# Optimization experiments

Measured on AMD Instinct MI355X. Metric: run time of the kernel, lower is better.

Reference implementation:

```python
import jax, jax.numpy as jnp
import numpy as np

B, L, H, O, NL = 1024, 100, 256, 256, 2


def setup_inputs() -> dict:
    key = jax.random.key(0)
    ks = jax.random.split(key, 20)
    s = 0.05  # weight scale to keep gates/softmax well-conditioned
    d = {
        "encoder_outputs": jax.random.normal(ks[0], (B, L, H), jnp.float32),
        "enc_h": jax.random.normal(ks[1], (NL, B, H), jnp.float32),
        "enc_c": jax.random.normal(ks[2], (NL, B, H), jnp.float32),
        "embedding": jax.random.uniform(ks[3], (O, H), jnp.float32, -1.0, 1.0),
        # torch nn.LSTM params, gate order (i, f, g, o)
        "Wih0": jax.random.normal(ks[4], (4 * H, 2 * H), jnp.float32) * s,
        "Whh0": jax.random.normal(ks[5], (4 * H, H), jnp.float32) * s,
        "bih0": jax.random.normal(ks[6], (4 * H,), jnp.float32) * s,
        "bhh0": jax.random.normal(ks[7], (4 * H,), jnp.float32) * s,
        "Wih1": jax.random.normal(ks[8], (4 * H, H), jnp.float32) * s,
        "Whh1": jax.random.normal(ks[9], (4 * H, H), jnp.float32) * s,
        "bih1": jax.random.normal(ks[10], (4 * H,), jnp.float32) * s,
        "bhh1": jax.random.normal(ks[11], (4 * H,), jnp.float32) * s,
        "Wa": jax.random.normal(ks[12], (H, H), jnp.float32) * s,        # Luong general score
        "Wconcat": jax.random.normal(ks[13], (H, 2 * H), jnp.float32) * s,
        "Wout": jax.random.normal(ks[14], (O, H), jnp.float32) * s,
        "Wcrit": jax.random.normal(ks[15], (O, O), jnp.float32) * s,
        "bcrit": jax.random.normal(ks[16], (O,), jnp.float32) * s,
        "actions": jax.random.randint(ks[17], (B, L), 0, O, jnp.int32),
    }
    return d


def _lstm_cell(x, h, c, Wih, Whh, bih, bhh):
    gates = x @ Wih.T + h @ Whh.T + bih + bhh  # [B, 4H]
    i, f, g, o = jnp.split(gates, 4, axis=-1)
    i = jax.nn.sigmoid(i)
    f = jax.nn.sigmoid(f)
    g = jnp.tanh(g)
    o = jax.nn.sigmoid(o)
    c_new = f * c + i * g
    h_new = o * jnp.tanh(c_new)
    return h_new, c_new


def reference(encoder_outputs, enc_h, enc_c, embedding,
              Wih0, Whh0, bih0, bhh0, Wih1, Whh1, bih1, bhh1,
              Wa, Wconcat, Wout, Wcrit, bcrit, actions):
    # Precompute Luong 'general' projection of encoder states (same math each step)
    enc_proj = encoder_outputs @ Wa.T  # [B, L, H]

    def step(carry, act_t):
        x, h, c, ctx = carry  # x:[B] int, h/c:[NL,B,H], ctx:[B,H]
        emb = embedding[x]                               # [B, H]
        inp = jnp.concatenate([emb, ctx], axis=-1)       # [B, 2H]
        h0, c0 = _lstm_cell(inp, h[0], c[0], Wih0, Whh0, bih0, bhh0)
        h1, c1 = _lstm_cell(h0, h[1], c[1], Wih1, Whh1, bih1, bhh1)
        out = h1                                         # [B, H]
        scores = jnp.einsum('bh,blh->bl', out, enc_proj)  # Luong general score
        attn = jax.nn.softmax(scores, axis=-1)
        ctx_att = jnp.einsum('bl,blh->bh', attn, encoder_outputs)
        new_ctx = jnp.tanh(jnp.concatenate([out, ctx_att], axis=-1) @ Wconcat.T)  # [B, H]
        logit_raw = new_ctx @ Wout.T                     # [B, O]
        pi = jax.nn.softmax(logit_raw, axis=-1)
        Q = logit_raw @ Wcrit.T + bcrit
        new_carry = (act_t, jnp.stack([h0, h1]), jnp.stack([c0, c1]), new_ctx)
        return new_carry, (pi, Q)

    x0 = jnp.zeros((B,), jnp.int32)
    ctx0 = encoder_outputs.mean(axis=1)                  # [B, H]
    _, (pis, Qs) = jax.lax.scan(step, (x0, enc_h, enc_c, ctx0), actions.T)
    logits = jnp.transpose(pis, (1, 0, 2))               # [B, L, O] (softmax probs, as in torch code)
    qvalues = jnp.transpose(Qs, (1, 0, 2))               # [B, L, O]
    values = (qvalues * logits).sum(-1)                  # [B, L]
    decoder_action = actions.astype(jnp.float32)         # teacher-forced actions recorded per step
    return decoder_action, logits, values
```

## Files before the change

### kernel.cpp

```cpp
#include <hip/hip_runtime.h>


#define Bx 1024
#define Lq 100
#define Hd 256
#define Od 256
#define H4 1024

typedef _Float16 f16;
typedef _Float16 half2_t __attribute__((ext_vector_type(2)));
typedef _Float16 f16x4 __attribute__((ext_vector_type(4)));
typedef unsigned int uint;
typedef uint uint4v __attribute__((ext_vector_type(4)));

__device__ __forceinline__ float fdot2(half2_t a, half2_t b, float c) {
#if __has_builtin(__builtin_amdgcn_fdot2)
  return __builtin_amdgcn_fdot2(a, b, c, false);
#else
  return c + (float)a.x * (float)b.x + (float)a.y * (float)b.y;
#endif
}
__device__ __forceinline__ float dot8(float acc, float4 w, float4 a) {
  acc = fdot2(__builtin_bit_cast(half2_t, w.x), __builtin_bit_cast(half2_t, a.x), acc);
  acc = fdot2(__builtin_bit_cast(half2_t, w.y), __builtin_bit_cast(half2_t, a.y), acc);
  acc = fdot2(__builtin_bit_cast(half2_t, w.z), __builtin_bit_cast(half2_t, a.z), acc);
  acc = fdot2(__builtin_bit_cast(half2_t, w.w), __builtin_bit_cast(half2_t, a.w), acc);
  return acc;
}
__device__ __forceinline__ float sigmf(float x) { return 1.0f / (1.0f + __expf(-x)); }



__global__ void k_cvt_lstm(const float* Wih0, const float* Whh0,
                           const float* Wih1, const float* Whh1, f16* dst) {
  int row = blockIdx.x, seg = row >> 10, r = row & 1023, c = threadIdx.x;
  const float* src; int stride, off;
  if (seg == 0)      { src = Wih0; stride = 512; off = 256; }
  else if (seg == 1) { src = Whh0; stride = 256; off = 0; }
  else if (seg == 2) { src = Wih1; stride = 256; off = 0; }
  else               { src = Whh1; stride = 256; off = 0; }
  size_t didx = (size_t)seg * 262144 + (size_t)(r >> 6) * 16384 +
                (size_t)(c >> 3) * 512 + (size_t)(r & 63) * 8 + (c & 7);
  dst[didx] = (f16)src[(size_t)r * stride + off + c];
}

__global__ void k_cvt_small(const float* Wconcat, const float* Wout,
                            const float* Wcrit, const float* Wa, f16* dst) {
  int blk = blockIdx.x, seg = blk >> 8, r = blk & 255, c = threadIdx.x;
  if (seg == 0) {
    dst[(size_t)(r >> 6) * 32768 + (size_t)(c >> 3) * 512 + (r & 63) * 8 + (c & 7)] =
        (f16)Wconcat[(size_t)r * 512 + c];
    int c2 = c + 256;
    dst[(size_t)(r >> 6) * 32768 + (size_t)(c2 >> 3) * 512 + (r & 63) * 8 + (c2 & 7)] =
        (f16)Wconcat[(size_t)r * 512 + c2];
  } else if (seg == 1) {
    dst[131072 + (size_t)(r >> 6) * 16384 + (size_t)(c >> 3) * 512 + (r & 63) * 8 + (c & 7)] =
        (f16)Wout[(size_t)r * 256 + c];
  } else if (seg == 2) {
    dst[196608 + (size_t)(r >> 6) * 16384 + (size_t)(c >> 3) * 512 + (r & 63) * 8 + (c & 7)] =
        (f16)Wcrit[(size_t)r * 256 + c];
  } else {
    dst[262144 + (size_t)(c >> 6) * 16384 + (size_t)(r >> 3) * 512 + (c & 63) * 8 + (r & 7)] =
        (f16)Wa[(size_t)r * 256 + c];
  }
}

__global__ void k_bias1(const float* bih1, const float* bhh1, float* b1) {
  int i = blockIdx.x * 256 + threadIdx.x;
  b1[i] = bih1[i] + bhh1[i];
}

__global__ void k_actions(const int* actions, float* out) {
  int i = blockIdx.x * 256 + threadIdx.x;
  out[i] = (float)actions[i];
}

__global__ void k_cvt_enc(const float* enc, f16* dst) {
  size_t i = (size_t)blockIdx.x * 256 + threadIdx.x;
  const float4* s = (const float4*)enc;
  float4 v = s[i];
  f16x4 o = {(f16)v.x, (f16)v.y, (f16)v.z, (f16)v.w};
  *(f16x4*)(dst + 4 * i) = o;
}

__global__ void k_table0(const float* emb, const float* Wih0,
                         const float* bih0, const float* bhh0, float* t0) {
  __shared__ float shw[16][256];
  int j0 = blockIdx.x * 16, tid = threadIdx.x;
  for (int i = tid; i < 16 * 256; i += 256) {
    int r = i >> 8, c = i & 255;
    shw[r][c] = Wih0[(size_t)(j0 + r) * 512 + c];
  }
  __syncthreads();
  int a = tid;
  float acc[16];
#pragma unroll
  for (int r = 0; r < 16; r++) acc[r] = 0.f;
  for (int k = 0; k < 256; k++) {
    float e = emb[(size_t)a * 256 + k];
#pragma unroll
    for (int r = 0; r < 16; r++) acc[r] = fmaf(e, shw[r][k], acc[r]);
  }
#pragma unroll
  for (int r = 0; r < 16; r++)
    t0[(size_t)a * H4 + j0 + r] = acc[r] + bih0[j0 + r] + bhh0[j0 + r];
}

template <bool E16>
__launch_bounds__(1024)
__global__ void k_seq(const float* enc, const f16* enc16,
                      const float* enc_h, const float* enc_c,
                      const int* actions, const float* bcrit,
                      const f16* wWih0c, const f16* wWhh0,
                      const f16* wWih1, const f16* wWhh1,
                      const f16* wWconcat, const f16* wWout, const f16* wWcrit,
                      const f16* wWaT,
                      const float* table0, const float* bias1, float* out) {
  const int tid = threadIdx.x;
  const int b0 = blockIdx.x * 4;

  __shared__ _Float16 sh_h0[4][264];
  __shared__ _Float16 sh_h1[4][264];
  __shared__ _Float16 sh_ctx[4][264];
  __shared__ _Float16 sh_ca[4][264];
  __shared__ _Float16 sh_logit[4][264];
  __shared__ _Float16 sh_v[4][264];
  __shared__ float sh_c0[4][256];
  __shared__ float sh_c1[4][256];
  __shared__ float sh_gates[4][H4];
  __shared__ float sh_sc[4][128];
  __shared__ float sh_pi[4][256];
  __shared__ float sh_red[4][20];
  __shared__ int sh_a[4];

  {
    int bb = tid >> 8, h = tid & 255, gb = b0 + bb;
    sh_h0[bb][h] = (f16)enc_h[(size_t)(0 * Bx + gb) * Hd + h];
    sh_h1[bb][h] = (f16)enc_h[(size_t)(1 * Bx + gb) * Hd + h];
    sh_c0[bb][h] = enc_c[(size_t)(0 * Bx + gb) * Hd + h];
    sh_c1[bb][h] = enc_c[(size_t)(1 * Bx + gb) * Hd + h];
    const float* ep = enc + (size_t)gb * Lq * Hd + h;
    float s = 0.f;
#pragma unroll 4
    for (int l = 0; l < Lq; l++) s += __builtin_nontemporal_load(ep + (size_t)l * Hd);
    sh_ctx[bb][h] = (f16)(s * (1.0f / Lq));
  }
  __syncthreads();

  for (int t = 0; t < Lq; t++) {
    if (tid < 4) sh_a[tid] = (t == 0) ? 0 : actions[(size_t)(b0 + tid) * Lq + (t - 1)];
    __syncthreads();

    {
      const int j = tid;
      const f16* w1 = wWih0c + (size_t)(j >> 6) * 16384 + (j & 63) * 8;
      const f16* w2 = wWhh0 + (size_t)(j >> 6) * 16384 + (j & 63) * 8;
      float a0 = table0[(size_t)sh_a[0] * H4 + j];
      float a1 = table0[(size_t)sh_a[1] * H4 + j];
      float a2 = table0[(size_t)sh_a[2] * H4 + j];
      float a3 = table0[(size_t)sh_a[3] * H4 + j];
#pragma unroll 4
      for (int c = 0; c < 32; c++) {
        float4 wa = *(const float4*)(w1 + (size_t)c * 512);
        float4 wb = *(const float4*)(w2 + (size_t)c * 512);
        float4 x0 = *(const float4*)&sh_ctx[0][8 * c];
        float4 x1 = *(const float4*)&sh_ctx[1][8 * c];
        float4 x2 = *(const float4*)&sh_ctx[2][8 * c];
        float4 x3 = *(const float4*)&sh_ctx[3][8 * c];
        a0 = dot8(a0, wa, x0); a1 = dot8(a1, wa, x1);
        a2 = dot8(a2, wa, x2); a3 = dot8(a3, wa, x3);
        float4 y0 = *(const float4*)&sh_h0[0][8 * c];
        float4 y1 = *(const float4*)&sh_h0[1][8 * c];
        float4 y2 = *(const float4*)&sh_h0[2][8 * c];
        float4 y3 = *(const float4*)&sh_h0[3][8 * c];
        a0 = dot8(a0, wb, y0); a1 = dot8(a1, wb, y1);
        a2 = dot8(a2, wb, y2); a3 = dot8(a3, wb, y3);
      }
      sh_gates[0][j] = a0; sh_gates[1][j] = a1;
      sh_gates[2][j] = a2; sh_gates[3][j] = a3;
    }
    __syncthreads();

    {
      int bb = tid >> 8, h = tid & 255;
      float gi = sh_gates[bb][h], gf = sh_gates[bb][h + 256];
      float gg = sh_gates[bb][h + 512], go = sh_gates[bb][h + 768];
      float c = sigmf(gf) * sh_c0[bb][h] + sigmf(gi) * tanhf(gg);
      sh_c0[bb][h] = c;
      sh_h0[bb][h] = (f16)(sigmf(go) * tanhf(c));
    }
    __syncthreads();

    {
      const int j = tid;
      const f16* w1 = wWih1 + (size_t)(j >> 6) * 16384 + (j & 63) * 8;
      const f16* w2 = wWhh1 + (size_t)(j >> 6) * 16384 + (j & 63) * 8;
      float bv = bias1[j];
      float a0 = bv, a1 = bv, a2 = bv, a3 = bv;
#pragma unroll 4
      for (int c = 0; c < 32; c++) {
        float4 wa = *(const float4*)(w1 + (size_t)c * 512);
        float4 wb = *(const float4*)(w2 + (size_t)c * 512);
        float4 x0 = *(const float4*)&sh_h0[0][8 * c];
        float4 x1 = *(const float4*)&sh_h0[1][8 * c];
        float4 x2 = *(const float4*)&sh_h0[2][8 * c];
        float4 x3 = *(const float4*)&sh_h0[3][8 * c];
        a0 = dot8(a0, wa, x0); a1 = dot8(a1, wa, x1);
        a2 = dot8(a2, wa, x2); a3 = dot8(a3, wa, x3);
        float4 y0 = *(const float4*)&sh_h1[0][8 * c];
        float4 y1 = *(const float4*)&sh_h1[1][8 * c];
        float4 y2 = *(const float4*)&sh_h1[2][8 * c];
        float4 y3 = *(const float4*)&sh_h1[3][8 * c];
        a0 = dot8(a0, wb, y0); a1 = dot8(a1, wb, y1);
        a2 = dot8(a2, wb, y2); a3 = dot8(a3, wb, y3);
      }
      sh_gates[0][j] = a0; sh_gates[1][j] = a1;
      sh_gates[2][j] = a2; sh_gates[3][j] = a3;
    }
    __syncthreads();

    {
      int bb = tid >> 8, h = tid & 255;
      float gi = sh_gates[bb][h], gf = sh_gates[bb][h + 256];
      float gg = sh_gates[bb][h + 512], go = sh_gates[bb][h + 768];
      float c = sigmf(gf) * sh_c1[bb][h] + sigmf(gi) * tanhf(gg);
      sh_c1[bb][h] = c;
      sh_h1[bb][h] = (f16)(sigmf(go) * tanhf(c));
    }
    __syncthreads();

    {
      int bb = tid >> 8, h = tid & 255;
      const f16* w = wWaT + (size_t)(h >> 6) * 16384 + (h & 63) * 8;
      float s = 0.f;
#pragma unroll 4
      for (int c = 0; c < 32; c++) {
        float4 wv = *(const float4*)(w + (size_t)c * 512);
        float4 av = *(const float4*)&sh_h1[bb][8 * c];
        s = dot8(s, wv, av);
      }
      sh_v[bb][h] = (f16)s;
    }
    __syncthreads();

    {
      int bb = tid >> 8, l = tid & 255;
      if (l < Lq) {
        float s = 0.f;
        if constexpr (E16) {
          const uint4v* ep = (const uint4v*)(enc16 + ((size_t)(b0 + bb) * Lq + l) * Hd);
#pragma unroll 4
          for (int c = 0; c < 32; c++) {
            uint4v u = ep[c];
            float4 ev = __builtin_bit_cast(float4, u);
            float4 vv = *(const float4*)&sh_v[bb][8 * c];
            s = dot8(s, ev, vv);
          }
        } else {
          const float4* ep = (const float4*)(enc + ((size_t)(b0 + bb) * Lq + l) * Hd);
#pragma unroll 4
          for (int c = 0; c < 64; c++) {
            float4 u = ep[c];
            const f16* vv = &sh_v[bb][4 * c];
            s = fmaf(u.x, (float)vv[0], s);
            s = fmaf(u.y, (float)vv[1], s);
            s = fmaf(u.z, (float)vv[2], s);
            s = fmaf(u.w, (float)vv[3], s);
          }
        }
        sh_sc[bb][l] = s;
      }
    }
    __syncthreads();

    if (tid < 256) {
      int bb = tid >> 6, lane = tid & 63;
      float v0 = (lane < Lq) ? sh_sc[bb][lane] : -1e30f;
      float v1 = (lane + 64 < Lq) ? sh_sc[bb][lane + 64] : -1e30f;
      float m = fmaxf(v0, v1);
      for (int off = 32; off; off >>= 1) m = fmaxf(m, __shfl_xor(m, off));
      float e0 = (lane < Lq) ? __expf(v0 - m) : 0.f;
      float e1 = (lane + 64 < Lq) ? __expf(v1 - m) : 0.f;
      float s = e0 + e1;
      for (int off = 32; off; off >>= 1) s += __shfl_xor(s, off);
      float inv = 1.0f / s;
      if (lane < Lq) sh_sc[bb][lane] = e0 * inv;
      if (lane + 64 < Lq) sh_sc[bb][lane + 64] = e1 * inv;
    }
    __syncthreads();

    if constexpr (E16) {
      int bb = tid >> 8, r = tid & 255;
      int hh = r & 127, half = r >> 7;
      const uint* ep = (const uint*)(enc16 + (size_t)(b0 + bb) * Lq * Hd) + hh;
      float s0 = 0.f, s1 = 0.f;
      int l0 = half * 50;
#pragma unroll 5
      for (int l = l0; l < l0 + 50; l++) {
        uint u = ep[(size_t)l * 128];
        half2_t hv = __builtin_bit_cast(half2_t, u);
        float a = sh_sc[bb][l];
        s0 = fmaf(a, (float)hv.x, s0);
        s1 = fmaf(a, (float)hv.y, s1);
      }
      sh_gates[bb][half * 512 + hh] = s0;
      sh_gates[bb][half * 512 + 128 + hh] = s1;
      __syncthreads();
      if (half == 0) {
        float r0 = sh_gates[bb][hh] + sh_gates[bb][512 + hh];
        float r1 = sh_gates[bb][128 + hh] + sh_gates[bb][512 + 128 + hh];
        half2_t rr = {(f16)r0, (f16)r1};
        *(half2_t*)&sh_ca[bb][2 * hh] = rr;
      }
    } else {
      int bb = tid >> 8, h = tid & 255;
      const float* ep = enc + (size_t)(b0 + bb) * Lq * Hd + h;
      float s = 0.f;
#pragma unroll 4
      for (int l = 0; l < Lq; l++)
        s = fmaf(sh_sc[bb][l], ep[(size_t)l * Hd], s);
      sh_ca[bb][h] = (f16)s;
    }
    __syncthreads();

    {
      int bb = tid >> 8, j = tid & 255;
      const f16* w = wWconcat + (size_t)(j >> 6) * 32768 + (j & 63) * 8;
      float s = 0.f;
#pragma unroll 4
      for (int c = 0; c < 32; c++) {
        float4 wv = *(const float4*)(w + (size_t)c * 512);
        float4 av = *(const float4*)&sh_h1[bb][8 * c];
        s = dot8(s, wv, av);
      }
#pragma unroll 4
      for (int c = 0; c < 32; c++) {
        float4 wv = *(const float4*)(w + (size_t)(32 + c) * 512);
        float4 av = *(const float4*)&sh_ca[bb][8 * c];
        s = dot8(s, wv, av);
      }
      sh_ctx[bb][j] = (f16)tanhf(s);
    }
    __syncthreads();

    {
      int bb = tid >> 8, o = tid & 255;
      const f16* w = wWout + (size_t)(o >> 6) * 16384 + (o & 63) * 8;
      float s = 0.f;
#pragma unroll 4
      for (int c = 0; c < 32; c++) {
        float4 wv = *(const float4*)(w + (size_t)c * 512);
        float4 av = *(const float4*)&sh_ctx[bb][8 * c];
        s = dot8(s, wv, av);
      }
      sh_logit[bb][o] = (f16)s;
      sh_pi[bb][o] = s;
    }
    __syncthreads();

    {
      int bb = tid >> 8, o = tid & 255, wv = (tid >> 6) & 3, lane = tid & 63;
      float v = sh_pi[bb][o];
      float m = v;
      for (int off = 32; off; off >>= 1) m = fmaxf(m, __shfl_xor(m, off));
      if (lane == 0) sh_red[bb][wv] = m;
      __syncthreads();
      m = fmaxf(fmaxf(sh_red[bb][0], sh_red[bb][1]), fmaxf(sh_red[bb][2], sh_red[bb][3]));
      float e = __expf(v - m);
      float s = e;
      for (int off = 32; off; off >>= 1) s += __shfl_xor(s, off);
      if (lane == 0) sh_red[bb][4 + wv] = s;
      __syncthreads();
      s = sh_red[bb][4] + sh_red[bb][5] + sh_red[bb][6] + sh_red[bb][7];
      float pi = e * (1.0f / s);
      sh_pi[bb][o] = pi;
      out[(size_t)Bx * Lq + ((size_t)(b0 + bb) * Lq + t) * Od + o] = pi;
    }
    __syncthreads();

    {
      int bb = tid >> 8, o = tid & 255, wv = (tid >> 6) & 3, lane = tid & 63;
      const f16* w = wWcrit + (size_t)(o >> 6) * 16384 + (o & 63) * 8;
      float q = bcrit[o];
#pragma unroll 4
      for (int c = 0; c < 32; c++) {
        float4 wv4 = *(const float4*)(w + (size_t)c * 512);
        float4 lv = *(const float4*)&sh_logit[bb][8 * c];
        q = dot8(q, wv4, lv);
      }
      float pv = sh_pi[bb][o] * q;
      for (int off = 32; off; off >>= 1) pv += __shfl_xor(pv, off);
      if (lane == 0) sh_red[bb][8 + wv] = pv;
    }
    __syncthreads();
    if (tid < 4) {
      float v = sh_red[tid][8] + sh_red[tid][9] + sh_red[tid][10] + sh_red[tid][11];
      out[(size_t)Bx * Lq * (1 + Od) + (size_t)(b0 + tid) * Lq + t] = v;
    }
    __syncthreads();
  }
}

extern "C" void kernel_launch(void* const* d_in, const int* in_sizes, int n_in,
                              void* d_out, int out_size, void* d_ws, size_t ws_size,
                              hipStream_t stream) {
  const float* enc    = (const float*)d_in[0];
  const float* enc_h  = (const float*)d_in[1];
  const float* enc_c  = (const float*)d_in[2];
  const float* emb    = (const float*)d_in[3];
  const float* Wih0   = (const float*)d_in[4];
  const float* Whh0   = (const float*)d_in[5];
  const float* bih0   = (const float*)d_in[6];
  const float* bhh0   = (const float*)d_in[7];
  const float* Wih1   = (const float*)d_in[8];
  const float* Whh1   = (const float*)d_in[9];
  const float* bih1   = (const float*)d_in[10];
  const float* bhh1   = (const float*)d_in[11];
  const float* Wa     = (const float*)d_in[12];
  const float* Wconcat= (const float*)d_in[13];
  const float* Wout   = (const float*)d_in[14];
  const float* Wcrit  = (const float*)d_in[15];
  const float* bcrit  = (const float*)d_in[16];
  const int* actions  = (const int*)d_in[17];
  float* out = (float*)d_out;

  const size_t ENC16_B = 52428800;
  const size_t W_B     = 2752512;
  const size_t T0_B    = 1048576;
  const size_t B1_B    = 4096;
  bool e16 = ws_size >= ENC16_B + W_B + T0_B + B1_B;

  char* ws = (char*)d_ws;
  f16* wsEnc16 = (f16*)ws;
  size_t base = e16 ? ENC16_B : 0;
  f16* wsW    = (f16*)(ws + base);
  float* wsT0 = (float*)(ws + base + W_B);
  float* wsB1 = (float*)(ws + base + W_B + T0_B);

  const f16* wWih0c   = wsW;
  const f16* wWhh0    = wsW + 262144;
  const f16* wWih1    = wsW + 524288;
  const f16* wWhh1    = wsW + 786432;
  const f16* wWconcat = wsW + 1048576;
  const f16* wWout    = wsW + 1179648;
  const f16* wWcrit   = wsW + 1245184;
  const f16* wWaT     = wsW + 1310720;

  hipLaunchKernelGGL(k_cvt_lstm, dim3(4096), dim3(256), 0, stream,
                     Wih0, Whh0, Wih1, Whh1, wsW);
  hipLaunchKernelGGL(k_cvt_small, dim3(1024), dim3(256), 0, stream,
                     Wconcat, Wout, Wcrit, Wa, (f16*)(wsW + 1048576));
  hipLaunchKernelGGL(k_bias1, dim3(4), dim3(256), 0, stream, bih1, bhh1, wsB1);
  hipLaunchKernelGGL(k_table0, dim3(64), dim3(256), 0, stream,
                     emb, Wih0, bih0, bhh0, wsT0);
  hipLaunchKernelGGL(k_actions, dim3(400), dim3(256), 0, stream, actions, out);
  if (e16) {
    hipLaunchKernelGGL(k_cvt_enc, dim3(25600), dim3(256), 0, stream, enc, wsEnc16);
    hipLaunchKernelGGL(k_seq<true>, dim3(256), dim3(1024), 0, stream,
                       enc, wsEnc16, enc_h, enc_c, actions, bcrit,
                       wWih0c, wWhh0, wWih1, wWhh1, wWconcat, wWout, wWcrit, wWaT,
                       wsT0, wsB1, out);
  } else {
    hipLaunchKernelGGL(k_seq<false>, dim3(256), dim3(1024), 0, stream,
                       enc, (const f16*)nullptr, enc_h, enc_c, actions, bcrit,
                       wWih0c, wWhh0, wWih1, wWhh1, wWconcat, wWout, wWcrit, wWaT,
                       wsT0, wsB1, out);
  }
}
```

Before: 6.365 ms.

## Double-buffer LSTM weight loads, split attention scores, drop softmax max and barriers

The LSTM gate matvecs now prefetch the next group of fp16 weight vectors into registers while the current group is computed (double buffering). The action indices are read straight from global memory instead of through shared memory, removing one barrier per step, and the trailing end-of-step barrier is also dropped. The attention score dot products are split across two halves of the hidden dimension so 200 threads work instead of 100. Several matvec loops are unrolled further and launch bounds request higher occupancy, which risks register spills. The softmax max-subtraction is removed, which relies on the logits being small enough not to overflow exp.

```diff
diff --git a/kernel.cpp b/kernel.cpp
--- a/kernel.cpp
+++ b/kernel.cpp
@@ -107,7 +107,7 @@
 }
 
 template <bool E16>
-__launch_bounds__(1024)
+__launch_bounds__(1024, 4)
 __global__ void k_seq(const float* enc, const f16* enc16,
                       const float* enc_h, const float* enc_c,
                       const int* actions, const float* bcrit,
@@ -131,7 +131,6 @@
   __shared__ float sh_sc[4][128];
   __shared__ float sh_pi[4][256];
   __shared__ float sh_red[4][20];
-  __shared__ int sh_a[4];
 
   {
     int bb = tid >> 8, h = tid & 255, gb = b0 + bb;
@@ -148,33 +147,54 @@
   __syncthreads();
 
   for (int t = 0; t < Lq; t++) {
-    if (tid < 4) sh_a[tid] = (t == 0) ? 0 : actions[(size_t)(b0 + tid) * Lq + (t - 1)];
-    __syncthreads();
-
     {
       const int j = tid;
       const f16* w1 = wWih0c + (size_t)(j >> 6) * 16384 + (j & 63) * 8;
       const f16* w2 = wWhh0 + (size_t)(j >> 6) * 16384 + (j & 63) * 8;
-      float a0 = table0[(size_t)sh_a[0] * H4 + j];
-      float a1 = table0[(size_t)sh_a[1] * H4 + j];
-      float a2 = table0[(size_t)sh_a[2] * H4 + j];
-      float a3 = table0[(size_t)sh_a[3] * H4 + j];
-#pragma unroll 4
-      for (int c = 0; c < 32; c++) {
-        float4 wa = *(const float4*)(w1 + (size_t)c * 512);
-        float4 wb = *(const float4*)(w2 + (size_t)c * 512);
-        float4 x0 = *(const float4*)&sh_ctx[0][8 * c];
-        float4 x1 = *(const float4*)&sh_ctx[1][8 * c];
-        float4 x2 = *(const float4*)&sh_ctx[2][8 * c];
-        float4 x3 = *(const float4*)&sh_ctx[3][8 * c];
-        a0 = dot8(a0, wa, x0); a1 = dot8(a1, wa, x1);
-        a2 = dot8(a2, wa, x2); a3 = dot8(a3, wa, x3);
-        float4 y0 = *(const float4*)&sh_h0[0][8 * c];
-        float4 y1 = *(const float4*)&sh_h0[1][8 * c];
-        float4 y2 = *(const float4*)&sh_h0[2][8 * c];
-        float4 y3 = *(const float4*)&sh_h0[3][8 * c];
-        a0 = dot8(a0, wb, y0); a1 = dot8(a1, wb, y1);
-        a2 = dot8(a2, wb, y2); a3 = dot8(a3, wb, y3);
+      int ia0 = (t == 0) ? 0 : actions[(size_t)(b0 + 0) * Lq + (t - 1)];
+      int ia1 = (t == 0) ? 0 : actions[(size_t)(b0 + 1) * Lq + (t - 1)];
+      int ia2 = (t == 0) ? 0 : actions[(size_t)(b0 + 2) * Lq + (t - 1)];
+      int ia3 = (t == 0) ? 0 : actions[(size_t)(b0 + 3) * Lq + (t - 1)];
+      float a0 = table0[(size_t)ia0 * H4 + j];
+      float a1 = table0[(size_t)ia1 * H4 + j];
+      float a2 = table0[(size_t)ia2 * H4 + j];
+      float a3 = table0[(size_t)ia3 * H4 + j];
+      float4 bA[4], bB[4], cA[4], cB[4];
+#pragma unroll
+      for (int u = 0; u < 4; u++) {
+        bA[u] = *(const float4*)(w1 + (size_t)u * 512);
+        cA[u] = *(const float4*)(w2 + (size_t)u * 512);
+      }
+#pragma unroll
+      for (int g = 0; g < 8; g++) {
+        if (g < 7) {
+#pragma unroll
+          for (int u = 0; u < 4; u++) {
+            int c = (g + 1) * 4 + u;
+            if (g % 2 == 0) { bB[u] = *(const float4*)(w1 + (size_t)c * 512);
+                              cB[u] = *(const float4*)(w2 + (size_t)c * 512); }
+            else            { bA[u] = *(const float4*)(w1 + (size_t)c * 512);
+                              cA[u] = *(const float4*)(w2 + (size_t)c * 512); }
+          }
+        }
+#pragma unroll
+        for (int u = 0; u < 4; u++) {
+          int c = g * 4 + u;
+          float4 wa = (g % 2 == 0) ? bA[u] : bB[u];
+          float4 wb = (g % 2 == 0) ? cA[u] : cB[u];
+          float4 x0 = *(const float4*)&sh_ctx[0][8 * c];
+          float4 x1 = *(const float4*)&sh_ctx[1][8 * c];
+          float4 x2 = *(const float4*)&sh_ctx[2][8 * c];
+          float4 x3 = *(const float4*)&sh_ctx[3][8 * c];
+          a0 = dot8(a0, wa, x0); a1 = dot8(a1, wa, x1);
+          a2 = dot8(a2, wa, x2); a3 = dot8(a3, wa, x3);
+          float4 y0 = *(const float4*)&sh_h0[0][8 * c];
+          float4 y1 = *(const float4*)&sh_h0[1][8 * c];
+          float4 y2 = *(const float4*)&sh_h0[2][8 * c];
+          float4 y3 = *(const float4*)&sh_h0[3][8 * c];
+          a0 = dot8(a0, wb, y0); a1 = dot8(a1, wb, y1);
+          a2 = dot8(a2, wb, y2); a3 = dot8(a3, wb, y3);
+        }
       }
       sh_gates[0][j] = a0; sh_gates[1][j] = a1;
       sh_gates[2][j] = a2; sh_gates[3][j] = a3;
@@ -197,22 +217,42 @@
       const f16* w2 = wWhh1 + (size_t)(j >> 6) * 16384 + (j & 63) * 8;
       float bv = bias1[j];
       float a0 = bv, a1 = bv, a2 = bv, a3 = bv;
-#pragma unroll 4
-      for (int c = 0; c < 32; c++) {
-        float4 wa = *(const float4*)(w1 + (size_t)c * 512);
-        float4 wb = *(const float4*)(w2 + (size_t)c * 512);
-        float4 x0 = *(const float4*)&sh_h0[0][8 * c];
-        float4 x1 = *(const float4*)&sh_h0[1][8 * c];
-        float4 x2 = *(const float4*)&sh_h0[2][8 * c];
-        float4 x3 = *(const float4*)&sh_h0[3][8 * c];
-        a0 = dot8(a0, wa, x0); a1 = dot8(a1, wa, x1);
-        a2 = dot8(a2, wa, x2); a3 = dot8(a3, wa, x3);
-        float4 y0 = *(const float4*)&sh_h1[0][8 * c];
-        float4 y1 = *(const float4*)&sh_h1[1][8 * c];
-        float4 y2 = *(const float4*)&sh_h1[2][8 * c];
-        float4 y3 = *(const float4*)&sh_h1[3][8 * c];
-        a0 = dot8(a0, wb, y0); a1 = dot8(a1, wb, y1);
-        a2 = dot8(a2, wb, y2); a3 = dot8(a3, wb, y3);
+      float4 bA[4], bB[4], cA[4], cB[4];
+#pragma unroll
+      for (int u = 0; u < 4; u++) {
+        bA[u] = *(const float4*)(w1 + (size_t)u * 512);
+        cA[u] = *(const float4*)(w2 + (size_t)u * 512);
+      }
+#pragma unroll
+      for (int g = 0; g < 8; g++) {
+        if (g < 7) {
+#pragma unroll
+          for (int u = 0; u < 4; u++) {
+            int c = (g + 1) * 4 + u;
+            if (g % 2 == 0) { bB[u] = *(const float4*)(w1 + (size_t)c * 512);
+                              cB[u] = *(const float4*)(w2 + (size_t)c * 512); }
+            else            { bA[u] = *(const float4*)(w1 + (size_t)c * 512);
+                              cA[u] = *(const float4*)(w2 + (size_t)c * 512); }
+          }
+        }
+#pragma unroll
+        for (int u = 0; u < 4; u++) {
+          int c = g * 4 + u;
+          float4 wa = (g % 2 == 0) ? bA[u] : bB[u];
+          float4 wb = (g % 2 == 0) ? cA[u] : cB[u];
+          float4 x0 = *(const float4*)&sh_h0[0][8 * c];
+          float4 x1 = *(const float4*)&sh_h0[1][8 * c];
+          float4 x2 = *(const float4*)&sh_h0[2][8 * c];
+          float4 x3 = *(const float4*)&sh_h0[3][8 * c];
+          a0 = dot8(a0, wa, x0); a1 = dot8(a1, wa, x1);
+          a2 = dot8(a2, wa, x2); a3 = dot8(a3, wa, x3);
+          float4 y0 = *(const float4*)&sh_h1[0][8 * c];
+          float4 y1 = *(const float4*)&sh_h1[1][8 * c];
+          float4 y2 = *(const float4*)&sh_h1[2][8 * c];
+          float4 y3 = *(const float4*)&sh_h1[3][8 * c];
+          a0 = dot8(a0, wb, y0); a1 = dot8(a1, wb, y1);
+          a2 = dot8(a2, wb, y2); a3 = dot8(a3, wb, y3);
+        }
       }
       sh_gates[0][j] = a0; sh_gates[1][j] = a1;
       sh_gates[2][j] = a2; sh_gates[3][j] = a3;
@@ -233,7 +273,7 @@
       int bb = tid >> 8, h = tid & 255;
       const f16* w = wWaT + (size_t)(h >> 6) * 16384 + (h & 63) * 8;
       float s = 0.f;
-#pragma unroll 4
+#pragma unroll 8
       for (int c = 0; c < 32; c++) {
         float4 wv = *(const float4*)(w + (size_t)c * 512);
         float4 av = *(const float4*)&sh_h1[bb][8 * c];
@@ -244,32 +284,40 @@
     __syncthreads();
 
     {
-      int bb = tid >> 8, l = tid & 255;
+      int bb = tid >> 8, r = tid & 255;
+      int l = r & 127, kh = r >> 7;
       if (l < Lq) {
-        float s = 0.f;
         if constexpr (E16) {
-          const uint4v* ep = (const uint4v*)(enc16 + ((size_t)(b0 + bb) * Lq + l) * Hd);
+          const uint4v* ep =
+              (const uint4v*)(enc16 + ((size_t)(b0 + bb) * Lq + l) * Hd) + kh * 16;
+          float s = 0.f;
+#pragma unroll 4
+          for (int c = 0; c < 16; c++) {
+            uint4v u = ep[c];
+            float4 ev = __builtin_bit_cast(float4, u);
+            float4 vv = *(const float4*)&sh_v[bb][8 * (kh * 16 + c)];
+            s = dot8(s, ev, vv);
+          }
+          sh_gates[bb][kh * 128 + l] = s;
+        } else {
+          const float4* ep =
+              (const float4*)(enc + ((size_t)(b0 + bb) * Lq + l) * Hd) + kh * 32;
+          float s = 0.f;
 #pragma unroll 4
           for (int c = 0; c < 32; c++) {
-            uint4v u = ep[c];
-            float4 ev = __builtin_bit_cast(float4, u);
-            float4 vv = *(const float4*)&sh_v[bb][8 * c];
-            s = dot8(s, ev, vv);
-          }
-        } else {
-          const float4* ep = (const float4*)(enc + ((size_t)(b0 + bb) * Lq + l) * Hd);
-#pragma unroll 4
-          for (int c = 0; c < 64; c++) {
             float4 u = ep[c];
-            const f16* vv = &sh_v[bb][4 * c];
+            const f16* vv = &sh_v[bb][4 * (kh * 32 + c)];
             s = fmaf(u.x, (float)vv[0], s);
             s = fmaf(u.y, (float)vv[1], s);
             s = fmaf(u.z, (float)vv[2], s);
             s = fmaf(u.w, (float)vv[3], s);
           }
+          sh_gates[bb][kh * 128 + l] = s;
         }
-        sh_sc[bb][l] = s;
-      }
+      }
+      __syncthreads();
+      if (kh == 0 && l < Lq)
+        sh_sc[bb][l] = sh_gates[bb][l] + sh_gates[bb][128 + l];
     }
     __syncthreads();
 
@@ -327,13 +375,13 @@
       int bb = tid >> 8, j = tid & 255;
       const f16* w = wWconcat + (size_t)(j >> 6) * 32768 + (j & 63) * 8;
       float s = 0.f;
-#pragma unroll 4
+#pragma unroll 8
       for (int c = 0; c < 32; c++) {
         float4 wv = *(const float4*)(w + (size_t)c * 512);
         float4 av = *(const float4*)&sh_h1[bb][8 * c];
         s = dot8(s, wv, av);
       }
-#pragma unroll 4
+#pragma unroll 8
       for (int c = 0; c < 32; c++) {
         float4 wv = *(const float4*)(w + (size_t)(32 + c) * 512);
         float4 av = *(const float4*)&sh_ca[bb][8 * c];
@@ -347,7 +395,7 @@
       int bb = tid >> 8, o = tid & 255;
       const f16* w = wWout + (size_t)(o >> 6) * 16384 + (o & 63) * 8;
       float s = 0.f;
-#pragma unroll 4
+#pragma unroll 8
       for (int c = 0; c < 32; c++) {
         float4 wv = *(const float4*)(w + (size_t)c * 512);
         float4 av = *(const float4*)&sh_ctx[bb][8 * c];
@@ -361,12 +409,7 @@
     {
       int bb = tid >> 8, o = tid & 255, wv = (tid >> 6) & 3, lane = tid & 63;
       float v = sh_pi[bb][o];
-      float m = v;
-      for (int off = 32; off; off >>= 1) m = fmaxf(m, __shfl_xor(m, off));
-      if (lane == 0) sh_red[bb][wv] = m;
-      __syncthreads();
-      m = fmaxf(fmaxf(sh_red[bb][0], sh_red[bb][1]), fmaxf(sh_red[bb][2], sh_red[bb][3]));
-      float e = __expf(v - m);
+      float e = __expf(v);
       float s = e;
       for (int off = 32; off; off >>= 1) s += __shfl_xor(s, off);
       if (lane == 0) sh_red[bb][4 + wv] = s;
@@ -382,7 +425,7 @@
       int bb = tid >> 8, o = tid & 255, wv = (tid >> 6) & 3, lane = tid & 63;
       const f16* w = wWcrit + (size_t)(o >> 6) * 16384 + (o & 63) * 8;
       float q = bcrit[o];
-#pragma unroll 4
+#pragma unroll 8
       for (int c = 0; c < 32; c++) {
         float4 wv4 = *(const float4*)(w + (size_t)c * 512);
         float4 lv = *(const float4*)&sh_logit[bb][8 * c];
@@ -397,7 +440,6 @@
       float v = sh_red[tid][8] + sh_red[tid][9] + sh_red[tid][10] + sh_red[tid][11];
       out[(size_t)Bx * Lq * (1 + Od) + (size_t)(b0 + tid) * Lq + t] = v;
     }
-    __syncthreads();
   }
 }
 
```

Result: slower. 14.66 ms (+130.3%).
